# Optimization experiments

Hardware: AMD Instinct MI355X
Metric: run time of the kernel (lower is better)

## Reference

```python
import jax, jax.numpy as jnp
import numpy as np
import math

D_MODEL = 1024
D_INNER = 2048
N_HEADS = 8
D_STATE = 64
D_CONV = 4
CHUNK = 64
HEAD_DIM = D_INNER // N_HEADS
EPS = 1.1920929e-07  # torch RMSNorm default eps = finfo(fp32).eps


def _rms(x, g):
    return x * jax.lax.rsqrt(jnp.mean(x * x, axis=-1, keepdims=True) + EPS) * g


def setup_inputs() -> dict:
    key = jax.random.key(0)
    ks = jax.random.split(key, 8)
    B, S = 32, 256
    proj_out = 2 * D_INNER + 2 * N_HEADS * D_STATE + N_HEADS  # 5128
    s = 0.02
    lambdas = [0.999, 0.995, 0.99, 0.98, 0.95, 0.9, 0.8, 0.7]
    A_log = jnp.log(jnp.asarray([-math.log(l) for l in lambdas], jnp.float32))
    return {
        "hidden": jax.random.normal(ks[0], (B, S, D_MODEL), jnp.float32),
        "W_in": jax.random.normal(ks[1], (proj_out, D_MODEL), jnp.float32) * s,
        "conv_w": jax.random.normal(ks[2], (D_INNER, 1, D_CONV), jnp.float32) * 0.2,
        "conv_b": jax.random.normal(ks[3], (D_INNER,), jnp.float32) * 0.02,
        "W_dt": jax.random.normal(ks[4], (D_INNER, N_HEADS), jnp.float32) * 0.1,
        "b_dt": jax.random.normal(ks[5], (D_INNER,), jnp.float32) * 0.1,
        "A_log": A_log,
        "D": jnp.ones((N_HEADS,), jnp.float32),
        "W_out": jax.random.normal(ks[6], (D_MODEL, D_INNER), jnp.float32) * s,
        "g_in": jnp.ones((D_MODEL,), jnp.float32),
        "g_out": jnp.ones((D_INNER,), jnp.float32),
    }


def reference(hidden, W_in, conv_w, conv_b, W_dt, b_dt, A_log, D, W_out, g_in, g_out):
    B, S, _ = hidden.shape
    residual = hidden
    h = _rms(hidden, g_in)
    proj = h @ W_in.T  # [B,S,5128]
    o1, o2 = D_INNER, 2 * D_INNER
    o3 = o2 + N_HEADS * D_STATE
    o4 = o3 + N_HEADS * D_STATE
    z = proj[..., :o1]
    x = proj[..., o1:o2]
    Bf = proj[..., o2:o3]
    Cf = proj[..., o3:o4]
    dt_raw = proj[..., o4:]
    # causal depthwise conv1d (pad left d_conv-1, trim to S)
    xt = jnp.transpose(x, (0, 2, 1))  # [B, d_inner, S]
    xc = jax.lax.conv_general_dilated(
        xt, conv_w, (1,), [(D_CONV - 1, 0)],
        feature_group_count=D_INNER, dimension_numbers=("NCH", "OIH", "NCH"))
    x = jax.nn.silu(jnp.transpose(xc + conv_b[None, :, None], (0, 2, 1)))
    # dt: project 8 -> d_inner then mean over head_dim -> per-head dt
    dt = dt_raw @ W_dt.T + b_dt  # [B,S,d_inner]
    dt_h = jax.nn.softplus(dt.reshape(B, S, N_HEADS, HEAD_DIM).mean(-1))  # non-TTT path (S<384)
    Bs = Bf.reshape(B, S, N_HEADS, D_STATE)
    Cs = Cf.reshape(B, S, N_HEADS, D_STATE)
    x_h = x.reshape(B, S, N_HEADS, HEAD_DIM)
    # chunked SSD scan
    A = -jnp.exp(A_log)  # [H]
    nC, L = S // CHUNK, CHUNK
    xck = x_h.reshape(B, nC, L, N_HEADS, HEAD_DIM)
    Bck = Bs.reshape(B, nC, L, N_HEADS, D_STATE)
    Cck = Cs.reshape(B, nC, L, N_HEADS, D_STATE)
    logA = dt_h.reshape(B, nC, L, N_HEADS) * A  # [B,c,L,H]
    lcs = jnp.cumsum(logA, axis=2)
    lcs_t = jnp.transpose(lcs, (0, 1, 3, 2))  # [B,c,H,L]
    tril = jnp.tril(jnp.ones((L, L), bool))
    M = jnp.where(tril, jnp.exp(lcs_t[..., :, None] - lcs_t[..., None, :]), 0.0)  # [B,c,H,L,L]
    # intra-chunk: sum_{s<=l,n} C[l,n] M[l,s] B[s,n] x[s,d]
    G = jnp.einsum("bclhn,bcshn->bchls", Cck, Bck)
    intra = jnp.einsum("bchls,bcshd->bclhd", G * M, xck)
    # per-chunk state contributions and decays
    Mlast = jnp.exp(lcs_t[..., -1:] - lcs_t)  # [B,c,H,L] decay from step s to chunk end
    states = jnp.einsum("bchs,bcshn,bcshd->bchdn", Mlast, Bck, xck)  # [B,c,H,hD,N]
    tdec = jnp.exp(lcs[:, :, -1, :])  # [B,c,H]
    def step(hst, inp):
        td, st = inp
        return td[..., None, None] * hst + st, hst
    init = jnp.zeros((B, N_HEADS, HEAD_DIM, D_STATE), x.dtype)
    _, h0 = jax.lax.scan(step, init, (jnp.moveaxis(tdec, 1, 0), jnp.moveaxis(states, 1, 0)))
    # inter-chunk: decay(l) * C[l] . h_start
    inter = jnp.exp(lcs)[..., None] * jnp.einsum("bclhn,cbhdn->bclhd", Cck, h0)
    y = (intra + inter).reshape(B, S, N_HEADS, HEAD_DIM) + x_h * D[None, None, :, None]
    y = y.reshape(B, S, D_INNER) * jax.nn.silu(z)
    y = _rms(y, g_out)
    return residual + y @ W_out.T
```

## Files before the change

kernel.cpp:

```cpp
#include <hip/hip_runtime.h>
#include <hip/hip_bf16.h>
#include <math.h>

typedef __hip_bfloat16 bf16;
typedef __attribute__((ext_vector_type(8))) short short8;
typedef __attribute__((ext_vector_type(4))) float f32x4;

#define AS1 __attribute__((address_space(1)))
#define AS3 __attribute__((address_space(3)))

#define D_MODEL 1024
#define D_INNER 2048
#define N_HEADS 8
#define D_STATE 64
#define CHUNK 64
#define HEAD_DIM 256
#define NCHUNK 4
#define BATCH 32
#define SEQ 256
#define ROWS (BATCH*SEQ)
#define PROJ_N 5128
#define PROJ_NPAD 5376
#define O1 D_INNER
#define O2 (2*D_INNER)
#define O3 (O2 + N_HEADS*D_STATE)
#define O4 (O3 + N_HEADS*D_STATE)
#define EPSF 1.1920929e-07f

__device__ __forceinline__ float silu_f(float x){ return x / (1.0f + expf(-x)); }
__device__ __forceinline__ float b2f(bf16 v){ return __bfloat162float(v); }
__device__ __forceinline__ bf16  f2b(float v){ return __float2bfloat16(v); }
__device__ __forceinline__ short f2s(float v){ bf16 b = __float2bfloat16(v); union{bf16 b; short s;} u; u.b=b; return u.s; }
__device__ __forceinline__ float s2f(short v){ union{short s; bf16 b;} u; u.s=v; return __bfloat162float(u.b); }

__device__ __forceinline__ void gl16(const void* g, void* l){
    __builtin_amdgcn_global_load_lds((const AS1 void*)g, (AS3 void*)l, 16, 0, 0);
}

__device__ __forceinline__ float block_sum_256(float v){
    __shared__ float sm[4];
    #pragma unroll
    for (int o = 32; o > 0; o >>= 1) v += __shfl_down(v, o, 64);
    int lane = threadIdx.x & 63, w = threadIdx.x >> 6;
    if (lane == 0) sm[w] = v;
    __syncthreads();
    return sm[0] + sm[1] + sm[2] + sm[3];
}

__global__ __launch_bounds__(256) void k_rms_in(const float* __restrict__ x,
                                                const float* __restrict__ g,
                                                bf16* __restrict__ out){
    int row = blockIdx.x, t = threadIdx.x;
    const float4* xr = (const float4*)(x + (size_t)row * D_MODEL);
    float4 v = xr[t];
    float ss = v.x*v.x + v.y*v.y + v.z*v.z + v.w*v.w;
    ss = block_sum_256(ss);
    float sc = rsqrtf(ss * (1.0f/(float)D_MODEL) + EPSF);
    float4 gv = ((const float4*)g)[t];
    union { ushort4 u; bf16 b[4]; } o;
    o.b[0] = f2b(v.x*sc*gv.x); o.b[1] = f2b(v.y*sc*gv.y);
    o.b[2] = f2b(v.z*sc*gv.z); o.b[3] = f2b(v.w*sc*gv.w);
    ((ushort4*)(out + (size_t)row * D_MODEL))[t] = o.u;
}

__global__ __launch_bounds__(256) void k_cvt_pad(const float* __restrict__ in,
                                                 bf16* __restrict__ out,
                                                 int n_in, int n_out){
    int i = (blockIdx.x * 256 + threadIdx.x) * 4;
    if (i >= n_out) return;
    union { ushort4 u; bf16 b[4]; } o;
    if (i + 3 < n_in){
        float4 v = *(const float4*)(in + i);
        o.b[0]=f2b(v.x); o.b[1]=f2b(v.y); o.b[2]=f2b(v.z); o.b[3]=f2b(v.w);
    } else {
        #pragma unroll
        for (int j = 0; j < 4; j++) o.b[j] = f2b((i+j < n_in) ? in[i+j] : 0.f);
    }
    *(ushort4*)(out + i) = o.u;
}


__device__ __forceinline__ short8 ld32(const short* base, int row, int g){
    int sr = row >> 1;
    int e8 = (((row & 1) << 2) | g) ^ (sr & 7);
    return *(const short8*)(base + sr*64 + e8*8);
}

__device__ __forceinline__ void stage_u(const bf16* __restrict__ Ag,
                                        const bf16* __restrict__ Bg,
                                        int K, size_t bm, size_t bn, int t,
                                        short* buf, int j){
    const int tid = threadIdx.x;
    const int wid = tid >> 6;
    int cidx = j*512 + tid;
    int srow = cidx >> 3, s8 = cidx & 7;
    int eff = s8 ^ (srow & 7);
    int grow = srow*2 + (eff >> 2);
    int gcol = t*32 + (eff & 3)*8;
    const bf16* src = (grow < 256)
        ? Ag + (bm + grow) * (size_t)K + gcol
        : Bg + (bn + grow - 256) * (size_t)K + gcol;
    gl16(src, buf + (size_t)(j*512 + wid*64)*8);
}

#define MFMA_BF16(A_,B_,C_) __builtin_amdgcn_mfma_f32_16x16x32_bf16(A_,B_,C_,0,0,0)

__device__ __forceinline__ void gemm_main(const bf16* __restrict__ Ag,
                                          const bf16* __restrict__ Bg,
                                          int K, size_t bm, size_t bn,
                                          short* lds, f32x4 (&acc)[4][4]){
    constexpr int TILE = 384*32;
    const int NT = K >> 5;
    const int lane = threadIdx.x & 63;
    const int wid = threadIdx.x >> 6;
    const int wm = wid >> 1, wn = wid & 1;
    const int fr = lane & 15, g = lane >> 4;

    #pragma unroll
    for (int j = 0; j < 3; j++) stage_u(Ag, Bg, K, bm, bn, 0, lds, j);
    #pragma unroll
    for (int j = 0; j < 3; j++) stage_u(Ag, Bg, K, bm, bn, 1, lds + TILE, j);
    asm volatile("s_waitcnt vmcnt(3)" ::: "memory");
    __builtin_amdgcn_sched_barrier(0);
    __builtin_amdgcn_s_barrier();
    __builtin_amdgcn_sched_barrier(0);

    int cur = 0;
    for (int t = 0; t < NT; t++){
        short* buf = lds + cur*TILE;
        int sg = cur + 2; if (sg >= 3) sg -= 3;
        short* stg = lds + sg*TILE;
        short8 a[4], b[4];
        #pragma unroll
        for (int m = 0; m < 4; m++) a[m] = ld32(buf, wm*64 + m*16 + fr, g);
        #pragma unroll
        for (int n = 0; n < 4; n++) b[n] = ld32(buf, 256 + wn*64 + n*16 + fr, g);
        if (t + 2 < NT){
            stage_u(Ag, Bg, K, bm, bn, t+2, stg, 0);
            stage_u(Ag, Bg, K, bm, bn, t+2, stg, 1);
            stage_u(Ag, Bg, K, bm, bn, t+2, stg, 2);
        }
        __builtin_amdgcn_s_setprio(1);
        #pragma unroll
        for (int m = 0; m < 4; m++)
            #pragma unroll
            for (int n = 0; n < 4; n++)
                acc[m][n] = MFMA_BF16(a[m], b[n], acc[m][n]);
        __builtin_amdgcn_s_setprio(0);
        __builtin_amdgcn_sched_barrier(0);
        if (t + 2 < NT)      asm volatile("s_waitcnt vmcnt(3)" ::: "memory");
        else if (t + 1 < NT) asm volatile("s_waitcnt vmcnt(0)" ::: "memory");
        __builtin_amdgcn_sched_barrier(0);
        __builtin_amdgcn_s_barrier();
        __builtin_amdgcn_sched_barrier(0);
        cur = cur + 1 == 3 ? 0 : cur + 1;
    }
}

__global__ __launch_bounds__(512, 4) void k_gemm1_g(const bf16* __restrict__ A,
                                                    const bf16* __restrict__ B,
                                                    bf16* __restrict__ z,
                                                    bf16* __restrict__ xp,
                                                    bf16* __restrict__ Bc,
                                                    bf16* __restrict__ Cc,
                                                    float* __restrict__ dtr){
    extern __shared__ short lds[];
    int wg = (blockIdx.x & 7)*168 + (blockIdx.x >> 3);
    int grp = wg / 192, rem = wg % 192;
    int nt_ = grp*6 + rem % 6;
    int mt_ = rem / 6;
    size_t bm = (size_t)mt_ * 256;
    size_t bn = (size_t)nt_ * 128;
    f32x4 acc[4][4] = {};
    gemm_main(A, B, D_MODEL, bm, bn, lds, acc);
    const int lane = threadIdx.x & 63;
    const int wid = threadIdx.x >> 6;
    const int wm = wid >> 1, wn = wid & 1;
    int cr = (lane >> 4)*4, cc = lane & 15;
    #pragma unroll
    for (int m = 0; m < 4; m++){
        size_t r0 = bm + wm*64 + m*16 + cr;
        #pragma unroll
        for (int n = 0; n < 4; n++){
            int c = (int)bn + wn*64 + n*16 + cc;
            #pragma unroll
            for (int j = 0; j < 4; j++){
                float v = acc[m][n][j];
                size_t r = r0 + j;
                if (c < O1)            z  [r * D_INNER + c]        = f2b(v);
                else if (c < O2)       xp [r * D_INNER + (c - O1)] = f2b(v);
                else if (c < O3)       Bc [r * 512 + (c - O2)]     = f2b(v);
                else if (c < O4)       Cc [r * 512 + (c - O3)]     = f2b(v);
                else if (c < PROJ_N)   dtr[r * 8 + (c - O4)]       = v;
            }
        }
    }
}

__global__ __launch_bounds__(512, 4) void k_gemm2_g(const bf16* __restrict__ A,
                                                    const bf16* __restrict__ B,
                                                    const float* __restrict__ res,
                                                    float* __restrict__ C){
    extern __shared__ short lds[];
    int wg = (blockIdx.x & 7)*32 + (blockIdx.x >> 3);
    size_t bm = (size_t)(wg >> 3) * 256;
    size_t bn = (size_t)(wg & 7) * 128;
    f32x4 acc[4][4] = {};
    gemm_main(A, B, D_INNER, bm, bn, lds, acc);
    const int lane = threadIdx.x & 63;
    const int wid = threadIdx.x >> 6;
    const int wm = wid >> 1, wn = wid & 1;
    int cr = (lane >> 4)*4, cc = lane & 15;
    #pragma unroll
    for (int m = 0; m < 4; m++){
        size_t r0 = bm + wm*64 + m*16 + cr;
        #pragma unroll
        for (int n = 0; n < 4; n++){
            size_t c = bn + wn*64 + n*16 + cc;
            #pragma unroll
            for (int j = 0; j < 4; j++){
                size_t r = r0 + j;
                C[r * D_MODEL + c] = acc[m][n][j] + res[r * D_MODEL + c];
            }
        }
    }
}

__global__ __launch_bounds__(256) void k_conv_silu(const bf16* __restrict__ xp,
                                                   const float* __restrict__ cw,
                                                   const float* __restrict__ cb,
                                                   bf16* __restrict__ xout){
    int b = blockIdx.x;
    int c = blockIdx.y * 256 + threadIdx.x;
    float w0 = cw[c*4+0], w1 = cw[c*4+1], w2 = cw[c*4+2], w3 = cw[c*4+3];
    float bias = cb[c];
    const bf16* ib = xp + (size_t)b * SEQ * D_INNER + c;
    bf16* ob = xout + (size_t)b * SEQ * D_INNER + c;
    float x0 = 0.f, x1 = 0.f, x2 = 0.f;
    for (int s = 0; s < SEQ; s++){
        float x3 = b2f(ib[(size_t)s * D_INNER]);
        float a = x0*w0 + x1*w1 + x2*w2 + x3*w3 + bias;
        ob[(size_t)s * D_INNER] = f2b(silu_f(a));
        x0 = x1; x1 = x2; x2 = x3;
    }
}

__global__ __launch_bounds__(64) void k_prep(const float* __restrict__ W_dt,
                                             const float* __restrict__ b_dt,
                                             const float* __restrict__ A_log,
                                             float* __restrict__ misc){
    int t = threadIdx.x;
    int h = t >> 3, k = t & 7;
    float s = 0.f;
    for (int d = 0; d < HEAD_DIM; d++) s += W_dt[(size_t)(h*HEAD_DIM + d) * N_HEADS + k];
    misc[t] = s * (1.0f/(float)HEAD_DIM);
    if (t < 8){
        float sb = 0.f;
        for (int d = 0; d < HEAD_DIM; d++) sb += b_dt[t*HEAD_DIM + d];
        misc[64 + t] = sb * (1.0f/(float)HEAD_DIM);
        misc[72 + t] = -expf(A_log[t]);
    }
}

__global__ __launch_bounds__(64) void k_dt_lcs(const float* __restrict__ dtr,
                                               const float* __restrict__ misc,
                                               float* __restrict__ lcs,
                                               float* __restrict__ tdec){
    __shared__ float sm[80];
    __shared__ float la[CHUNK][N_HEADS];
    int bc = blockIdx.x;
    int l = threadIdx.x;
    for (int i = l; i < 80; i += 64) sm[i] = misc[i];
    __syncthreads();
    const float* dr = dtr + (size_t)(bc*CHUNK + l) * 8;
    float d0 = dr[0], d1 = dr[1], d2 = dr[2], d3 = dr[3];
    float d4 = dr[4], d5 = dr[5], d6 = dr[6], d7 = dr[7];
    #pragma unroll
    for (int h = 0; h < 8; h++){
        float dt = sm[64+h]
                 + d0*sm[h*8+0] + d1*sm[h*8+1] + d2*sm[h*8+2] + d3*sm[h*8+3]
                 + d4*sm[h*8+4] + d5*sm[h*8+5] + d6*sm[h*8+6] + d7*sm[h*8+7];
        float sp = (dt > 20.f) ? dt : log1pf(expf(dt));
        la[l][h] = sp * sm[72+h];
    }
    __syncthreads();
    float out[8];
    #pragma unroll
    for (int h = 0; h < 8; h++) out[h] = 0.f;
    for (int l2 = 0; l2 <= l; l2++){
        #pragma unroll
        for (int h = 0; h < 8; h++) out[h] += la[l2][h];
    }
    float* lo = lcs + (size_t)(bc*CHUNK + l) * N_HEADS;
    #pragma unroll
    for (int h = 0; h < 8; h++) lo[h] = out[h];
    if (l == 63){
        #pragma unroll
        for (int h = 0; h < 8; h++) tdec[bc*N_HEADS + h] = expf(out[h]);
    }
}

#define LB   0
#define LC   4096
#define LGM  8192
#define LXT  12800
#define LSH  29184
#define LF   45568
#define LDS_BYTES 91904

__device__ __forceinline__ short8 frag_sw(const short* arr, int r, int k){
    return *(const short8*)(arr + r*64 + (k ^ ((r&7)<<3)));
}

__global__ __launch_bounds__(256, 1) void k_ssm(const bf16* __restrict__ Bc,
                                                const bf16* __restrict__ Cc,
                                                bf16* xg,
                                                const float* __restrict__ lcs,
                                                const float* __restrict__ tdec,
                                                const float* __restrict__ Dv){
    extern __shared__ short lds[];
    short* Blds  = lds + LB;
    short* Clds  = lds + LC;
    short* GMlds = lds + LGM;
    short* XTlds = lds + LXT;
    short* Shr   = lds + LSH;
    float* el = (float*)(lds + LF);
    float* ml = el + 64;
    float* ee = el + 128;

    const int tid = threadIdx.x;
    const int lane = tid & 63;
    const int wid = tid >> 6;
    const int fr = lane & 15;
    const int fk = (lane >> 4) * 8;
    const int r0 = (lane >> 4) * 4;
    const int b = blockIdx.x >> 3, h = blockIdx.x & 7;
    const float Dh = Dv[h];

    f32x4 carry[4][4] = {};

    for (int c = 0; c < NCHUNK; c++){
        const int bc = b*NCHUNK + c;
        __syncthreads();
        #pragma unroll
        for (int i = 0; i < 2; i++){
            int slot = i*256 + tid;
            int s = slot >> 3, u = slot & 7;
            size_t rb = (size_t)(bc*CHUNK + s) * 512 + h*64 + ((u ^ (s&7)) * 8);
            gl16(Bc + rb, Blds + slot*8);
            gl16(Cc + rb, Clds + slot*8);
        }
        #pragma unroll
        for (int i = 0; i < 8; i++){
            int slot = i*256 + tid;
            int s = slot >> 5, ck = slot & 31;
            gl16(xg + (size_t)(bc*CHUNK + s) * D_INNER + h*HEAD_DIM + ck*8, Shr + slot*8);
        }
        if (tid < 64) el[tid] = lcs[(size_t)(bc*CHUNK + tid) * N_HEADS + h];
        __syncthreads();
        if (tid < 64){
            float e63 = el[63];
            ml[tid] = expf(e63 - el[tid]);
            ee[tid] = expf(el[tid]);
        }
        #pragma unroll
        for (int i = 0; i < 8; i++){
            short8 t8;
            #pragma unroll
            for (int j = 0; j < 8; j++) t8[j] = Shr[(i*8 + j)*HEAD_DIM + tid];
            *(short8*)(XTlds + tid*64 + ((i*8) ^ ((tid&7)<<3))) = t8;
        }
        __syncthreads();
        {
            f32x4 accg[4] = {};
            #pragma unroll
            for (int kk = 0; kk < 2; kk++){
                short8 a = frag_sw(Clds, wid*16 + fr, kk*32 + fk);
                #pragma unroll
                for (int nt = 0; nt < 4; nt++){
                    short8 bb = frag_sw(Blds, nt*16 + fr, kk*32 + fk);
                    accg[nt] = __builtin_amdgcn_mfma_f32_16x16x32_bf16(a, bb, accg[nt], 0, 0, 0);
                }
            }
            #pragma unroll
            for (int nt = 0; nt < 4; nt++){
                int s = nt*16 + fr;
                float els = el[s];
                #pragma unroll
                for (int j = 0; j < 4; j++){
                    int l = wid*16 + r0 + j;
                    float f = (s <= l) ? expf(el[l] - els) : 0.f;
                    GMlds[l*72 + s] = f2s(accg[nt][j] * f);
                }
            }
            int crow = wid*16 + (lane >> 2), cq = lane & 3;
            float fe = ee[crow];
            #pragma unroll
            for (int half = 0; half < 2; half++){
                short8 v = *(short8*)(Clds + crow*64 + cq*16 + half*8);
                #pragma unroll
                for (int j = 0; j < 8; j++) v[j] = f2s(s2f(v[j]) * fe);
                *(short8*)(Clds + crow*64 + cq*16 + half*8) = v;
            }
        }
        #pragma unroll
        for (int mt = 0; mt < 4; mt++)
            #pragma unroll
            for (int nt = 0; nt < 4; nt++)
                #pragma unroll
                for (int j = 0; j < 4; j++){
                    int d = wid*64 + mt*16 + r0 + j;
                    int n = nt*16 + fr;
                    Shr[d*64 + (n ^ ((d&7)<<3))] = f2s(carry[mt][nt][j]);
                }
        float btv[16];
        {
            int bn_ = tid & 63, bq = tid >> 6;
            #pragma unroll
            for (int i = 0; i < 16; i++){
                int s = bq*16 + i;
                btv[i] = s2f(Blds[s*64 + (bn_ ^ ((s&7)<<3))]) * ml[s];
            }
        }
        __syncthreads();
        {
            int bn_ = tid & 63, bq = tid >> 6;
            #pragma unroll
            for (int i = 0; i < 16; i++){
                int s = bq*16 + i;
                Blds[bn_*64 + (s ^ ((bn_&7)<<3))] = f2s(btv[i]);
            }
        }
        {
            f32x4 accy[4][4] = {};
            #pragma unroll
            for (int kk = 0; kk < 2; kk++){
                short8 ag[4], ae[4], bx[4], bh[4];
                #pragma unroll
                for (int mt = 0; mt < 4; mt++){
                    ag[mt] = *(const short8*)(GMlds + (mt*16 + fr)*72 + kk*32 + fk);
                    ae[mt] = frag_sw(Clds, mt*16 + fr, kk*32 + fk);
                }
                #pragma unroll
                for (int nt = 0; nt < 4; nt++){
                    int d = wid*64 + nt*16 + fr;
                    bx[nt] = frag_sw(XTlds, d, kk*32 + fk);
                    bh[nt] = frag_sw(Shr,  d, kk*32 + fk);
                }
                #pragma unroll
                for (int mt = 0; mt < 4; mt++)
                    #pragma unroll
                    for (int nt = 0; nt < 4; nt++){
                        accy[mt][nt] = __builtin_amdgcn_mfma_f32_16x16x32_bf16(ag[mt], bx[nt], accy[mt][nt], 0, 0, 0);
                        accy[mt][nt] = __builtin_amdgcn_mfma_f32_16x16x32_bf16(ae[mt], bh[nt], accy[mt][nt], 0, 0, 0);
                    }
            }
            #pragma unroll
            for (int mt = 0; mt < 4; mt++)
                #pragma unroll
                for (int nt = 0; nt < 4; nt++){
                    int d = wid*64 + nt*16 + fr;
                    #pragma unroll
                    for (int j = 0; j < 4; j++){
                        int l = mt*16 + r0 + j;
                        float xv = s2f(XTlds[d*64 + (l ^ ((d&7)<<3))]);
                        xg[(size_t)(bc*CHUNK + l) * D_INNER + h*HEAD_DIM + d] = f2b(accy[mt][nt][j] + xv*Dh);
                    }
                }
        }
        __syncthreads();
        {
            f32x4 accs[4][4] = {};
            #pragma unroll
            for (int kk = 0; kk < 2; kk++){
                short8 ax[4], bt[4];
                #pragma unroll
                for (int mt = 0; mt < 4; mt++)
                    ax[mt] = frag_sw(XTlds, wid*64 + mt*16 + fr, kk*32 + fk);
                #pragma unroll
                for (int nt = 0; nt < 4; nt++)
                    bt[nt] = frag_sw(Blds, nt*16 + fr, kk*32 + fk);
                #pragma unroll
                for (int mt = 0; mt < 4; mt++)
                    #pragma unroll
                    for (int nt = 0; nt < 4; nt++)
                        accs[mt][nt] = __builtin_amdgcn_mfma_f32_16x16x32_bf16(ax[mt], bt[nt], accs[mt][nt], 0, 0, 0);
            }
            float td = tdec[bc*N_HEADS + h];
            #pragma unroll
            for (int mt = 0; mt < 4; mt++)
                #pragma unroll
                for (int nt = 0; nt < 4; nt++)
                    carry[mt][nt] = td * carry[mt][nt] + accs[mt][nt];
        }
    }
}

__global__ __launch_bounds__(256) void k_gate_rms(const bf16* __restrict__ y,
                                                  const bf16* __restrict__ z,
                                                  const float* __restrict__ g,
                                                  bf16* __restrict__ yn){
    int row = blockIdx.x, t = threadIdx.x;
    union { uint4 u; bf16 b[8]; } yv, zv, ov;
    yv.u = ((const uint4*)(y + (size_t)row * D_INNER))[t];
    zv.u = ((const uint4*)(z + (size_t)row * D_INNER))[t];
    float v[8];
    float ss = 0.f;
    #pragma unroll
    for (int i = 0; i < 8; i++){
        float a = b2f(yv.b[i]);
        float q = b2f(zv.b[i]);
        v[i] = a * silu_f(q);
        ss += v[i]*v[i];
    }
    ss = block_sum_256(ss);
    float sc = rsqrtf(ss * (1.0f/(float)D_INNER) + EPSF);
    const float4* g4 = (const float4*)g;
    float4 ga = g4[2*t], gb = g4[2*t+1];
    float gg[8] = {ga.x,ga.y,ga.z,ga.w,gb.x,gb.y,gb.z,gb.w};
    #pragma unroll
    for (int i = 0; i < 8; i++) ov.b[i] = f2b(v[i]*sc*gg[i]);
    ((uint4*)(yn + (size_t)row * D_INNER))[t] = ov.u;
}

extern "C" void kernel_launch(void* const* d_in, const int* in_sizes, int n_in,
                              void* d_out, int out_size, void* d_ws, size_t ws_size,
                              hipStream_t stream){
    const float* hidden = (const float*)d_in[0];
    const float* W_in   = (const float*)d_in[1];
    const float* conv_w = (const float*)d_in[2];
    const float* conv_b = (const float*)d_in[3];
    const float* W_dt   = (const float*)d_in[4];
    const float* b_dt   = (const float*)d_in[5];
    const float* A_log  = (const float*)d_in[6];
    const float* Dv     = (const float*)d_in[7];
    const float* W_out  = (const float*)d_in[8];
    const float* g_in   = (const float*)d_in[9];
    const float* g_out  = (const float*)d_in[10];

    char* ws = (char*)d_ws;
    bf16*  z    = (bf16*)(ws + 0);
    bf16*  xp   = (bf16*)(ws + 33554432);
    bf16*  x    = (bf16*)(ws + 67108864);
    bf16*  Bc   = (bf16*)(ws + 100663296);
    bf16*  Cc   = (bf16*)(ws + 109051904);
    float* dtr  = (float*)(ws + 117440512);
    float* lcs  = (float*)(ws + 117702656);
    float* tdec = (float*)(ws + 117964800);
    float* misc = (float*)(ws + 117968896);
    bf16*  Wb   = (bf16*)(ws + 117969408);
    bf16*  hnb  = (bf16*)(ws + 128979456);
    bf16*  yn   = xp;

    k_rms_in<<<ROWS, 256, 0, stream>>>(hidden, g_in, hnb);
    k_cvt_pad<<<(PROJ_NPAD*D_MODEL/4 + 255)/256, 256, 0, stream>>>(W_in, Wb, PROJ_N*D_MODEL, PROJ_NPAD*D_MODEL);
    hipFuncSetAttribute((const void*)k_gemm1_g, hipFuncAttributeMaxDynamicSharedMemorySize, 73728);
    k_gemm1_g<<<(ROWS/256)*(PROJ_NPAD/128), 512, 73728, stream>>>(hnb, Wb, z, xp, Bc, Cc, dtr);
    k_conv_silu<<<dim3(BATCH, D_INNER/256), 256, 0, stream>>>(xp, conv_w, conv_b, x);
    k_prep<<<1, 64, 0, stream>>>(W_dt, b_dt, A_log, misc);
    k_dt_lcs<<<BATCH*NCHUNK, 64, 0, stream>>>(dtr, misc, lcs, tdec);
    hipFuncSetAttribute((const void*)k_ssm, hipFuncAttributeMaxDynamicSharedMemorySize, LDS_BYTES);
    k_ssm<<<BATCH*N_HEADS, 256, LDS_BYTES, stream>>>(Bc, Cc, x, lcs, tdec, Dv);
    k_gate_rms<<<ROWS, 256, 0, stream>>>(x, z, g_out, yn);
    k_cvt_pad<<<(D_MODEL*D_INNER/4 + 255)/256, 256, 0, stream>>>(W_out, Wb, D_MODEL*D_INNER, D_MODEL*D_INNER);
    hipFuncSetAttribute((const void*)k_gemm2_g, hipFuncAttributeMaxDynamicSharedMemorySize, 73728);
    k_gemm2_g<<<(ROWS/256)*(D_MODEL/128), 512, 73728, stream>>>(yn, Wb, hidden, (float*)d_out);
}
```

Measured before the change: 287.6 us.

## Switch input-projection GEMM to double-buffered LDS pipeline for higher occupancy

The first GEMM now uses a new main loop with two LDS tile buffers instead of three. Loads for tile t+2 are issued into the buffer just consumed, after a barrier. This cuts dynamic LDS from 72 KB to 48 KB and raises the launch-bounds occupancy hint from 4 to 6, so more workgroups can sit on each CU. In exchange, each iteration needs an extra barrier and loses the deeper prefetch distance, so latency hiding per block may get worse.

```diff
diff --git a/kernel.cpp b/kernel.cpp
--- a/kernel.cpp
+++ b/kernel.cpp
@@ -105,6 +105,57 @@
 
 #define MFMA_BF16(A_,B_,C_) __builtin_amdgcn_mfma_f32_16x16x32_bf16(A_,B_,C_,0,0,0)
 
+__device__ __forceinline__ void gemm_main_r2(const bf16* __restrict__ Ag,
+                                             const bf16* __restrict__ Bg,
+                                             int K, size_t bm, size_t bn,
+                                             short* lds, f32x4 (&acc)[4][4]){
+    constexpr int TILE = 384*32;
+    const int NT = K >> 5;
+    const int lane = threadIdx.x & 63;
+    const int wid = threadIdx.x >> 6;
+    const int wm = wid >> 1, wn = wid & 1;
+    const int fr = lane & 15, g = lane >> 4;
+
+    #pragma unroll
+    for (int j = 0; j < 3; j++) stage_u(Ag, Bg, K, bm, bn, 0, lds, j);
+    #pragma unroll
+    for (int j = 0; j < 3; j++) stage_u(Ag, Bg, K, bm, bn, 1, lds + TILE, j);
+    asm volatile("s_waitcnt vmcnt(3)" ::: "memory");
+    __builtin_amdgcn_sched_barrier(0);
+    __builtin_amdgcn_s_barrier();
+    __builtin_amdgcn_sched_barrier(0);
+
+    for (int t = 0; t < NT; t++){
+        short* buf = lds + (t & 1)*TILE;
+        short8 a[4], b[4];
+        #pragma unroll
+        for (int m = 0; m < 4; m++) a[m] = ld32(buf, wm*64 + m*16 + fr, g);
+        #pragma unroll
+        for (int n = 0; n < 4; n++) b[n] = ld32(buf, 256 + wn*64 + n*16 + fr, g);
+        __builtin_amdgcn_s_setprio(1);
+        #pragma unroll
+        for (int m = 0; m < 4; m++)
+            #pragma unroll
+            for (int n = 0; n < 4; n++)
+                acc[m][n] = MFMA_BF16(a[m], b[n], acc[m][n]);
+        __builtin_amdgcn_s_setprio(0);
+        __builtin_amdgcn_sched_barrier(0);
+        __builtin_amdgcn_s_barrier();
+        __builtin_amdgcn_sched_barrier(0);
+        if (t + 2 < NT){
+            stage_u(Ag, Bg, K, bm, bn, t+2, buf, 0);
+            stage_u(Ag, Bg, K, bm, bn, t+2, buf, 1);
+            stage_u(Ag, Bg, K, bm, bn, t+2, buf, 2);
+            asm volatile("s_waitcnt vmcnt(3)" ::: "memory");
+        } else if (t + 1 < NT){
+            asm volatile("s_waitcnt vmcnt(0)" ::: "memory");
+        }
+        __builtin_amdgcn_sched_barrier(0);
+        __builtin_amdgcn_s_barrier();
+        __builtin_amdgcn_sched_barrier(0);
+    }
+}
+
 __device__ __forceinline__ void gemm_main(const bf16* __restrict__ Ag,
                                           const bf16* __restrict__ Bg,
                                           int K, size_t bm, size_t bn,
@@ -157,7 +208,7 @@
     }
 }
 
-__global__ __launch_bounds__(512, 4) void k_gemm1_g(const bf16* __restrict__ A,
+__global__ __launch_bounds__(512, 6) void k_gemm1_g(const bf16* __restrict__ A,
                                                     const bf16* __restrict__ B,
                                                     bf16* __restrict__ z,
                                                     bf16* __restrict__ xp,
@@ -172,7 +223,7 @@
     size_t bm = (size_t)mt_ * 256;
     size_t bn = (size_t)nt_ * 128;
     f32x4 acc[4][4] = {};
-    gemm_main(A, B, D_MODEL, bm, bn, lds, acc);
+    gemm_main_r2(A, B, D_MODEL, bm, bn, lds, acc);
     const int lane = threadIdx.x & 63;
     const int wid = threadIdx.x >> 6;
     const int wm = wid >> 1, wn = wid & 1;
@@ -554,8 +605,8 @@
 
     k_rms_in<<<ROWS, 256, 0, stream>>>(hidden, g_in, hnb);
     k_cvt_pad<<<(PROJ_NPAD*D_MODEL/4 + 255)/256, 256, 0, stream>>>(W_in, Wb, PROJ_N*D_MODEL, PROJ_NPAD*D_MODEL);
-    hipFuncSetAttribute((const void*)k_gemm1_g, hipFuncAttributeMaxDynamicSharedMemorySize, 73728);
-    k_gemm1_g<<<(ROWS/256)*(PROJ_NPAD/128), 512, 73728, stream>>>(hnb, Wb, z, xp, Bc, Cc, dtr);
+    hipFuncSetAttribute((const void*)k_gemm1_g, hipFuncAttributeMaxDynamicSharedMemorySize, 49152);
+    k_gemm1_g<<<(ROWS/256)*(PROJ_NPAD/128), 512, 49152, stream>>>(hnb, Wb, z, xp, Bc, Cc, dtr);
     k_conv_silu<<<dim3(BATCH, D_INNER/256), 256, 0, stream>>>(xp, conv_w, conv_b, x);
     k_prep<<<1, 64, 0, stream>>>(W_dt, b_dt, A_log, misc);
     k_dt_lcs<<<BATCH*NCHUNK, 64, 0, stream>>>(dtr, misc, lcs, tdec);
```

Measured after the change: 1.135 ms. 295% more time.
